# Kernel optimization log

Measured on AMD Instinct MI355X. Metric: run time of the kernel, lower is better.

The kernel has to match this reference:

```python
import jax, jax.numpy as jnp
import numpy as np

B, T, EMB, H = 4, 2048, 1024, 16
S = EMB // H


def setup_inputs() -> dict:
    key = jax.random.key(0)
    ks = jax.random.split(key, 7)
    x = jax.random.normal(ks[0], (B, T, EMB), dtype=jnp.float32)
    pad_amounts = jax.random.randint(ks[1], (B,), 0, 512, dtype=jnp.int64)
    Wk = jax.random.normal(ks[2], (S, S), dtype=jnp.float32) * (1.0 / np.sqrt(S))
    Wq = jax.random.normal(ks[3], (S, S), dtype=jnp.float32) * (1.0 / np.sqrt(S))
    Wv = jax.random.normal(ks[4], (S, S), dtype=jnp.float32) * (1.0 / np.sqrt(S))
    Wu = jax.random.normal(ks[5], (EMB, EMB), dtype=jnp.float32) * (1.0 / np.sqrt(EMB))
    bu = jax.random.normal(ks[6], (EMB,), dtype=jnp.float32) * 0.01
    return {"x": x, "Wk": Wk, "Wq": Wq, "Wv": Wv, "Wu": Wu, "bu": bu,
            "pad_amounts": pad_amounts}


def reference(x, Wk, Wq, Wv, Wu, bu, pad_amounts):
    b, t, e = x.shape
    h = H
    s = e // h
    xh = x.reshape(b, t, h, s)
    # torch Linear: y = x @ W.T (no bias for k/q/v)
    keys = jnp.einsum('bths,os->btho', xh, Wk)
    queries = jnp.einsum('bths,os->btho', xh, Wq)
    values = jnp.einsum('bths,os->btho', xh, Wv)
    # (b,t,h,s) -> (b*h,t,s)
    keys = keys.transpose(0, 2, 1, 3).reshape(b * h, t, s)
    queries = queries.transpose(0, 2, 1, 3).reshape(b * h, t, s)
    values = values.transpose(0, 2, 1, 3).reshape(b * h, t, s)
    scale = e ** 0.25
    queries = queries / scale
    keys = keys / scale
    dot = jnp.einsum('nqs,nks->nqk', queries, keys)  # (b*h, t, t)
    # Faithful to original bug: only the first b flat indices of b*h get masked.
    pad_full = jnp.concatenate([pad_amounts,
                                jnp.zeros(b * h - b, dtype=pad_amounts.dtype)])
    thresh = (t - pad_full)[:, None, None]  # (b*h,1,1); thresh=t -> no mask
    pos = jnp.arange(t)
    mask = (pos[None, :, None] >= thresh) & (pos[None, None, :] >= thresh)
    dot = jnp.where(mask, -jnp.inf, dot)
    att = jax.nn.softmax(dot, axis=2)
    out = jnp.einsum('nqk,nks->nqs', att, values)  # (b*h,t,s)
    out = out.reshape(b, h, t, s).transpose(0, 2, 1, 3).reshape(b, t, h * s)
    return out @ Wu.T + bu
```

## Files before the change

kernel.cpp:

```cpp
#include <hip/hip_runtime.h>


typedef float f32x4 __attribute__((ext_vector_type(4)));
typedef float f32x16 __attribute__((ext_vector_type(16)));
typedef _Float16 f16x2 __attribute__((ext_vector_type(2)));
typedef _Float16 f16x8 __attribute__((ext_vector_type(8)));
typedef unsigned u32x4 __attribute__((ext_vector_type(4)));

#define MFMA16(a, b, c) __builtin_amdgcn_mfma_f32_16x16x32_f16((a), (b), (c), 0, 0, 0)
#define MFMA32(a, b, c) __builtin_amdgcn_mfma_f32_32x32x16_f16((a), (b), (c), 0, 0, 0)

constexpr int Tn = 2048;
constexpr int Bn = 4;
constexpr int EMBn = 1024;
constexpr float NEG_INF = -3.0e38f;

__device__ __forceinline__ float exp2_hw(float x) {
  float r; asm("v_exp_f32 %0, %1" : "=v"(r) : "v"(x)); return r;
}
__device__ __forceinline__ unsigned pkrtz(float lo, float hi) {
  unsigned r; asm("v_cvt_pkrtz_f16_f32 %0, %1, %2" : "=v"(r) : "v"(lo), "v"(hi)); return r;
}
__device__ __forceinline__ unsigned pkadd(unsigned a, unsigned b) {
  unsigned r; asm("v_pk_add_f16 %0, %1, %2" : "=v"(r) : "v"(a), "v"(b)); return r;
}
__device__ __forceinline__ void permswap(unsigned& a, unsigned& b) {
  asm("v_permlane32_swap_b32 %0, %1" : "+v"(a), "+v"(b));
}

__global__ __launch_bounds__(256) void sa_prep(
    const float* __restrict__ Wk, const float* __restrict__ Wq,
    const float* __restrict__ Wv, const float* __restrict__ Wu,
    _Float16* __restrict__ w3, _Float16* __restrict__ wub) {
  int idx = blockIdx.x * 256 + threadIdx.x;
  const float rs = 0.21233046f;
  if (idx < 1048576) wub[idx] = (_Float16)Wu[idx];
  if (idx < 4096) {
    w3[idx]        = (_Float16)(Wk[idx] * rs);
    w3[4096 + idx] = (_Float16)(Wq[idx] * rs);
    w3[8192 + idx] = (_Float16)(Wv[idx]);
  }
}

__global__ __launch_bounds__(256) void sa_qkv(
    const float* __restrict__ x, const _Float16* __restrict__ w3,
    _Float16* __restrict__ Qb, _Float16* __restrict__ Kb, _Float16* __restrict__ Vt) {
  const int wave = threadIdx.x >> 6;
  const int lane = threadIdx.x & 63;
  const int g = lane >> 4, c = lane & 15;
  const int n = blockIdx.y, b = n >> 4, h = n & 15;
  const int t0 = blockIdx.x * 64 + wave * 16;

  f16x8 ax[2];
#pragma unroll
  for (int kk = 0; kk < 2; ++kk) {
    const float* xp = x + ((long)((b * Tn + t0 + c) * 16 + h)) * 64 + kk * 32 + g * 8;
    f32x4 u = *(const f32x4*)xp;
    f32x4 v = *(const f32x4*)(xp + 4);
    f16x8 a;
    a[0] = (_Float16)u[0]; a[1] = (_Float16)u[1]; a[2] = (_Float16)u[2]; a[3] = (_Float16)u[3];
    a[4] = (_Float16)v[0]; a[5] = (_Float16)v[1]; a[6] = (_Float16)v[2]; a[7] = (_Float16)v[3];
    ax[kk] = a;
  }

#pragma unroll
  for (int w = 0; w < 2; ++w) {
    _Float16* dst = w ? Qb : Kb;
#pragma unroll
    for (int ot = 0; ot < 4; ++ot) {
      f32x4 a_ = {0.f, 0.f, 0.f, 0.f};
#pragma unroll
      for (int kk = 0; kk < 2; ++kk) {
        f16x8 wf = *(const f16x8*)(w3 + w * 4096 + (ot * 16 + c) * 64 + kk * 32 + g * 8);
        a_ = MFMA16(ax[kk], wf, a_);
      }
#pragma unroll
      for (int r = 0; r < 4; ++r)
        dst[((long)n * Tn + t0 + g * 4 + r) * 64 + ot * 16 + c] = (_Float16)a_[r];
    }
  }

#pragma unroll
  for (int ot = 0; ot < 4; ++ot) {
    f32x4 a_ = {0.f, 0.f, 0.f, 0.f};
#pragma unroll
    for (int kk = 0; kk < 2; ++kk) {
      f16x8 wf = *(const f16x8*)(w3 + 8192 + (ot * 16 + c) * 64 + kk * 32 + g * 8);
      a_ = MFMA16(wf, ax[kk], a_);
    }
#pragma unroll
    for (int r = 0; r < 4; ++r)
      Vt[((long)n * 64 + ot * 16 + g * 4 + r) * Tn + t0 + c] = (_Float16)a_[r];
  }
}

__global__ __launch_bounds__(256, 2) void sa_flash(
    const _Float16* __restrict__ Qb, const _Float16* __restrict__ Kb,
    const _Float16* __restrict__ Vt, const int* __restrict__ pad32,
    _Float16* __restrict__ AO) {
  const int bid = blockIdx.x;
  const int n = (bid & 7) * 8 + (bid >> 6);
  const int qblk = (bid >> 3) & 7;
  const int tid = threadIdx.x;
  const int wave = tid >> 6;
  const int lane = tid & 63;
  const int ql = lane & 31;
  const int hi = lane >> 5;

  int thresh = Tn;
  if (n < Bn) {
    bool is64 = (pad32[1] == 0 && pad32[3] == 0);
    int pv = is64 ? pad32[2 * n] : pad32[n];
    thresh = Tn - pv;
  }

  const int qbase = qblk * 256 + wave * 64;
  const _Float16* Qh = Qb + (long)n * Tn * 64;
  const _Float16* Kh = Kb + (long)n * Tn * 64;
  const _Float16* Vh = Vt + (long)n * 64 * Tn;

  f16x8 bq[2][4];
#pragma unroll
  for (int qh = 0; qh < 2; ++qh) {
    const _Float16* qp = Qh + (long)(qbase + qh * 32 + ql) * 64 + hi * 8;
#pragma unroll
    for (int ks = 0; ks < 4; ++ks) bq[qh][ks] = *(const f16x8*)(qp + ks * 16);
  }

  __shared__ __align__(16) char smem[36864];

  const int sr = tid >> 2, sc = tid & 3;
  const _Float16* kgp = Kh + sr * 64 + sc * 8;
  const _Float16* vgp = Vh + (long)sr * Tn + sc * 8;
  char* kw = smem + sr * 144 + sc * 16;
  char* vw = smem + 18432 + sr * 144 + sc * 16;

  f32x16 o[2][2];
  f32x16 zf;
#pragma unroll
  for (int i = 0; i < 16; ++i) {
    o[0][0][i] = 0.f; o[0][1][i] = 0.f; o[1][0][i] = 0.f; o[1][1][i] = 0.f;
    zf[i] = 0.f;
  }
  float l0 = 0.f, l1 = 0.f;

  const bool qge0 = (qbase + ql) >= thresh;
  const bool qge1 = (qbase + 32 + ql) >= thresh;
  const bool qany = (qbase + 64) > thresh;

  {
    f16x8 k0 = *(const f16x8*)kgp;
    f16x8 k1 = *(const f16x8*)(kgp + 32);
    f16x8 v0 = *(const f16x8*)vgp;
    f16x8 v1 = *(const f16x8*)(vgp + 32);
    *(f16x8*)kw = k0;
    *(f16x8*)(kw + 64) = k1;
    *(f16x8*)vw = v0;
    *(f16x8*)(vw + 64) = v1;
  }
  __syncthreads();

  int cur = 0;
  for (int kb = 0; kb < Tn; kb += 64) {
    const int kbn = (kb + 64) & (Tn - 1);
    f16x8 kst0 = *(const f16x8*)(kgp + kbn * 64);
    f16x8 kst1 = *(const f16x8*)(kgp + kbn * 64 + 32);
    f16x8 vst0 = *(const f16x8*)(vgp + kbn);
    f16x8 vst1 = *(const f16x8*)(vgp + kbn + 32);

    const char* kbb = smem + cur * 9216;
    const char* vbb = smem + 18432 + cur * 9216;

#pragma unroll
    for (int sub = 0; sub < 2; ++sub) {
      const char* krow = kbb + (sub * 32 + ql) * 144 + hi * 16;
      f16x8 ka0 = *(const f16x8*)(krow);
      f16x8 ka1 = *(const f16x8*)(krow + 32);
      f16x8 ka2 = *(const f16x8*)(krow + 64);
      f16x8 ka3 = *(const f16x8*)(krow + 96);

      __builtin_amdgcn_s_setprio(1);
      f32x16 st0 = MFMA32(ka0, bq[0][0], zf);
      f32x16 st1 = MFMA32(ka0, bq[1][0], zf);
      st0 = MFMA32(ka1, bq[0][1], st0);
      st1 = MFMA32(ka1, bq[1][1], st1);
      st0 = MFMA32(ka2, bq[0][2], st0);
      st1 = MFMA32(ka2, bq[1][2], st1);
      st0 = MFMA32(ka3, bq[0][3], st0);
      st1 = MFMA32(ka3, bq[1][3], st1);
      __builtin_amdgcn_s_setprio(0);

      if (qany && (kb + sub * 32 + 32) > thresh) {
#pragma unroll
        for (int r = 0; r < 16; ++r) {
          int kr_ = kb + sub * 32 + (r & 3) + 8 * (r >> 2) + 4 * hi;
          if (kr_ >= thresh) {
            if (qge0) st0[r] = NEG_INF;
            if (qge1) st1[r] = NEG_INF;
          }
        }
      }

      const char* vrow0 = vbb + ql * 144 + sub * 64 + hi * 16;
      const char* vrow1 = vrow0 + 32 * 144;
      f16x8 va0 = *(const f16x8*)(vrow0);
      f16x8 va1 = *(const f16x8*)(vrow0 + 32);
      f16x8 va2 = *(const f16x8*)(vrow1);
      f16x8 va3 = *(const f16x8*)(vrow1 + 32);

#pragma unroll
      for (int qh = 0; qh < 2; ++qh) {
        const f32x16& stq = qh ? st1 : st0;
        float p[16];
#pragma unroll
        for (int r = 0; r < 16; ++r) p[r] = exp2_hw(stq[r]);

        unsigned pw[8], psum[2];
#pragma unroll
        for (int j = 0; j < 2; ++j) {
          unsigned a0 = pkrtz(p[j * 8 + 0], p[j * 8 + 1]);
          unsigned b0 = pkrtz(p[j * 8 + 4], p[j * 8 + 5]);
          unsigned a1 = pkrtz(p[j * 8 + 2], p[j * 8 + 3]);
          unsigned b1 = pkrtz(p[j * 8 + 6], p[j * 8 + 7]);
          psum[j] = pkadd(pkadd(a0, b0), pkadd(a1, b1));
          permswap(a0, b0);
          permswap(a1, b1);
          pw[j * 4 + 0] = a0; pw[j * 4 + 1] = a1;
          pw[j * 4 + 2] = b0; pw[j * 4 + 3] = b1;
        }
        {
          f16x2 ph = __builtin_bit_cast(f16x2, pkadd(psum[0], psum[1]));
          if (qh) l1 += (float)ph[0] + (float)ph[1];
          else    l0 += (float)ph[0] + (float)ph[1];
        }
        u32x4 u0 = {pw[0], pw[1], pw[2], pw[3]};
        u32x4 u1 = {pw[4], pw[5], pw[6], pw[7]};
        f16x8 pb0 = __builtin_bit_cast(f16x8, u0);
        f16x8 pb1 = __builtin_bit_cast(f16x8, u1);

        __builtin_amdgcn_s_setprio(1);
        o[qh][0] = MFMA32(va0, pb0, o[qh][0]);
        o[qh][0] = MFMA32(va1, pb1, o[qh][0]);
        o[qh][1] = MFMA32(va2, pb0, o[qh][1]);
        o[qh][1] = MFMA32(va3, pb1, o[qh][1]);
        __builtin_amdgcn_s_setprio(0);
      }
    }

    char* kwd = kw + (cur ^ 1) * 9216;
    char* vwd = vw + (cur ^ 1) * 9216;
    *(f16x8*)kwd = kst0;
    *(f16x8*)(kwd + 64) = kst1;
    *(f16x8*)vwd = vst0;
    *(f16x8*)(vwd + 64) = vst1;
    __syncthreads();
    cur ^= 1;
  }

  float lf0 = l0 + __shfl_xor(l0, 32, 64);
  float lf1 = l1 + __shfl_xor(l1, 32, 64);
  float linv0 = 1.0f / lf0;
  float linv1 = 1.0f / lf1;

  const int bb = n >> 4, hh = n & 15;
  const int qr = lane >> 3, s0 = (lane & 7) * 8;
  _Float16* my = (_Float16*)(smem + wave * 8192);
#pragma unroll
  for (int qh = 0; qh < 2; ++qh) {
    float linv = qh ? linv1 : linv0;
    _Float16* myq = my + qh * 2048;
#pragma unroll
    for (int stile = 0; stile < 2; ++stile) {
#pragma unroll
      for (int r = 0; r < 16; r += 2) {
        unsigned wv = pkrtz(o[qh][stile][r] * linv, o[qh][stile][r + 1] * linv);
        int s = stile * 32 + (r & 3) + 8 * (r >> 2) + 4 * hi;
        *(unsigned*)(myq + ql * 64 + (s ^ ((ql & 7) << 3))) = wv;
      }
    }
  }
  asm volatile("s_waitcnt lgkmcnt(0)" ::: "memory");

#pragma unroll
  for (int qh = 0; qh < 2; ++qh) {
    _Float16* myq = my + qh * 2048;
#pragma unroll
    for (int j = 0; j < 4; ++j) {
      int q = j * 8 + qr;
      f16x8 vv = *(const f16x8*)(myq + q * 64 + (s0 ^ ((q & 7) << 3)));
      *(f16x8*)(AO + ((long)(bb * Tn + qbase + qh * 32 + q)) * EMBn + hh * 64 + s0) = vv;
    }
  }
}

__global__ __launch_bounds__(256, 4) void sa_oproj(
    const _Float16* __restrict__ A, const _Float16* __restrict__ WuB,
    const float* __restrict__ bu, float* __restrict__ Y) {
  const int bid = blockIdx.x;
  const int xcd = bid & 7;
  const int j = bid >> 3;
  const int nstrip = j & 15;
  const int mblk = xcd * 8 + (j >> 4);
  const int tid = threadIdx.x;
  const int wave = tid >> 6;
  const int lane = tid & 63;
  const int ql = lane & 31;
  const int hi = lane >> 5;
  const int mbase = mblk * 128 + wave * 32;
  const int nbase = nstrip * 64;

  __shared__ __align__(16) char bsm[18432];
  const int sr = tid >> 3, sc = tid & 7;
  const _Float16* wg0 = WuB + (long)(nbase + sr) * 1024 + sc * 8;
  const _Float16* wg1 = WuB + (long)(nbase + sr + 32) * 1024 + sc * 8;
  char* ww0 = bsm + sr * 144 + sc * 16;
  char* ww1 = bsm + (sr + 32) * 144 + sc * 16;

  const _Float16* ap = A + (long)(mbase + ql) * 1024 + hi * 8;

  f32x16 acc[2];
#pragma unroll
  for (int i = 0; i < 16; ++i) { acc[0][i] = 0.f; acc[1][i] = 0.f; }

  {
    f16x8 w0 = *(const f16x8*)wg0;
    f16x8 w1 = *(const f16x8*)wg1;
    *(f16x8*)ww0 = w0;
    *(f16x8*)ww1 = w1;
  }
  __syncthreads();

  int cur = 0;
  for (int kb = 0; kb < 1024; kb += 64) {
    const int kbn = (kb + 64) & 1023;
    f16x8 wn0 = *(const f16x8*)(wg0 + kbn);
    f16x8 wn1 = *(const f16x8*)(wg1 + kbn);

    f16x8 af[4];
#pragma unroll
    for (int ks = 0; ks < 4; ++ks) af[ks] = *(const f16x8*)(ap + kb + ks * 16);

    const char* bbase = bsm + cur * 9216;
#pragma unroll
    for (int nt = 0; nt < 2; ++nt) {
      const char* brow = bbase + (nt * 32 + ql) * 144;
#pragma unroll
      for (int ks = 0; ks < 4; ++ks) {
        f16x8 bf = *(const f16x8*)(brow + (ks * 2 + hi) * 16);
        acc[nt] = MFMA32(af[ks], bf, acc[nt]);
      }
    }

    *(f16x8*)(ww0 + (cur ^ 1) * 9216) = wn0;
    *(f16x8*)(ww1 + (cur ^ 1) * 9216) = wn1;
    __syncthreads();
    cur ^= 1;
  }

#pragma unroll
  for (int nt = 0; nt < 2; ++nt) {
    float bias = bu[nbase + nt * 32 + ql];
#pragma unroll
    for (int r = 0; r < 16; ++r) {
      int mrow = mbase + (r & 3) + 8 * (r >> 2) + 4 * hi;
      Y[(long)mrow * 1024 + nbase + nt * 32 + ql] = acc[nt][r] + bias;
    }
  }
}

extern "C" void kernel_launch(void* const* d_in, const int* in_sizes, int n_in,
                              void* d_out, int out_size, void* d_ws, size_t ws_size,
                              hipStream_t stream) {
  const float* x  = (const float*)d_in[0];
  const float* Wk = (const float*)d_in[1];
  const float* Wq = (const float*)d_in[2];
  const float* Wv = (const float*)d_in[3];
  const float* Wu = (const float*)d_in[4];
  const float* bu = (const float*)d_in[5];
  const int* pad  = (const int*)d_in[6];
  float* Y = (float*)d_out;

  _Float16* ws  = (_Float16*)d_ws;
  _Float16* w3  = ws;
  _Float16* wub = ws + 16384;
  _Float16* Qb  = ws + 16384 + 1048576;
  _Float16* Kb  = Qb + 8388608;
  _Float16* Vt  = Kb + 8388608;
  _Float16* AO  = Vt + 8388608;

  sa_prep<<<4096, 256, 0, stream>>>(Wk, Wq, Wv, Wu, w3, wub);
  sa_qkv<<<dim3(32, 64), 256, 0, stream>>>(x, w3, Qb, Kb, Vt);
  sa_flash<<<dim3(512), 256, 0, stream>>>(Qb, Kb, Vt, pad, AO);
  sa_oproj<<<dim3(1024), 256, 0, stream>>>(AO, wub, bu, Y);
}
```

Baseline: 148.0 us.

## Stream K/V tiles into LDS with direct global-to-LDS loads and XOR swizzle

```diff
diff --git a/kernel.cpp b/kernel.cpp
--- a/kernel.cpp
+++ b/kernel.cpp
@@ -26,6 +26,11 @@
 }
 __device__ __forceinline__ void permswap(unsigned& a, unsigned& b) {
   asm("v_permlane32_swap_b32 %0, %1" : "+v"(a), "+v"(b));
+}
+__device__ __forceinline__ void glds16(const void* g, void* l) {
+  __builtin_amdgcn_global_load_lds(
+      (const __attribute__((address_space(1))) unsigned*)g,
+      (__attribute__((address_space(3))) unsigned*)l, 16, 0, 0);
 }
 
 __global__ __launch_bounds__(256) void sa_prep(
@@ -127,13 +132,12 @@
     for (int ks = 0; ks < 4; ++ks) bq[qh][ks] = *(const f16x8*)(qp + ks * 16);
   }
 
-  __shared__ __align__(16) char smem[36864];
-
-  const int sr = tid >> 2, sc = tid & 3;
-  const _Float16* kgp = Kh + sr * 64 + sc * 8;
-  const _Float16* vgp = Vh + (long)sr * Tn + sc * 8;
-  char* kw = smem + sr * 144 + sc * 16;
-  char* vw = smem + 18432 + sr * 144 + sc * 16;
+  __shared__ __align__(16) char smem[32768];
+
+  const int srow = wave * 16 + (lane >> 3);
+  const int sswz = ((lane & 7) ^ (lane >> 3)) * 8;
+  const _Float16* ksrc = Kh + (long)srow * 64 + sswz;
+  const _Float16* vsrc = Vh + (long)srow * Tn + sswz;
 
   f32x16 o[2][2];
   f32x16 zf;
@@ -147,37 +151,40 @@
   const bool qge0 = (qbase + ql) >= thresh;
   const bool qge1 = (qbase + 32 + ql) >= thresh;
   const bool qany = (qbase + 64) > thresh;
+  const int sw = ql & 7;
 
   {
-    f16x8 k0 = *(const f16x8*)kgp;
-    f16x8 k1 = *(const f16x8*)(kgp + 32);
-    f16x8 v0 = *(const f16x8*)vgp;
-    f16x8 v1 = *(const f16x8*)(vgp + 32);
-    *(f16x8*)kw = k0;
-    *(f16x8*)(kw + 64) = k1;
-    *(f16x8*)vw = v0;
-    *(f16x8*)(vw + 64) = v1;
+    char* kd = smem + wave * 2048;
+    char* vd = smem + 16384 + wave * 2048;
+    glds16(ksrc, kd);
+    glds16(ksrc + 512, kd + 1024);
+    glds16(vsrc, vd);
+    glds16(vsrc + 8 * Tn, vd + 1024);
   }
   __syncthreads();
 
   int cur = 0;
   for (int kb = 0; kb < Tn; kb += 64) {
     const int kbn = (kb + 64) & (Tn - 1);
-    f16x8 kst0 = *(const f16x8*)(kgp + kbn * 64);
-    f16x8 kst1 = *(const f16x8*)(kgp + kbn * 64 + 32);
-    f16x8 vst0 = *(const f16x8*)(vgp + kbn);
-    f16x8 vst1 = *(const f16x8*)(vgp + kbn + 32);
-
-    const char* kbb = smem + cur * 9216;
-    const char* vbb = smem + 18432 + cur * 9216;
+    {
+      char* kd = smem + (cur ^ 1) * 8192 + wave * 2048;
+      char* vd = smem + 16384 + (cur ^ 1) * 8192 + wave * 2048;
+      glds16(ksrc + kbn * 64, kd);
+      glds16(ksrc + kbn * 64 + 512, kd + 1024);
+      glds16(vsrc + kbn, vd);
+      glds16(vsrc + kbn + 8 * Tn, vd + 1024);
+    }
+
+    const char* kbb = smem + cur * 8192;
+    const char* vbb = smem + 16384 + cur * 8192;
 
 #pragma unroll
     for (int sub = 0; sub < 2; ++sub) {
-      const char* krow = kbb + (sub * 32 + ql) * 144 + hi * 16;
-      f16x8 ka0 = *(const f16x8*)(krow);
-      f16x8 ka1 = *(const f16x8*)(krow + 32);
-      f16x8 ka2 = *(const f16x8*)(krow + 64);
-      f16x8 ka3 = *(const f16x8*)(krow + 96);
+      const char* krow = kbb + (sub * 32 + ql) * 128;
+      f16x8 ka0 = *(const f16x8*)(krow + (((0 + hi) ^ sw) * 16));
+      f16x8 ka1 = *(const f16x8*)(krow + (((2 + hi) ^ sw) * 16));
+      f16x8 ka2 = *(const f16x8*)(krow + (((4 + hi) ^ sw) * 16));
+      f16x8 ka3 = *(const f16x8*)(krow + (((6 + hi) ^ sw) * 16));
 
       __builtin_amdgcn_s_setprio(1);
       f32x16 st0 = MFMA32(ka0, bq[0][0], zf);
@@ -201,12 +208,12 @@
         }
       }
 
-      const char* vrow0 = vbb + ql * 144 + sub * 64 + hi * 16;
-      const char* vrow1 = vrow0 + 32 * 144;
-      f16x8 va0 = *(const f16x8*)(vrow0);
-      f16x8 va1 = *(const f16x8*)(vrow0 + 32);
-      f16x8 va2 = *(const f16x8*)(vrow1);
-      f16x8 va3 = *(const f16x8*)(vrow1 + 32);
+      const char* vrow0 = vbb + ql * 128;
+      const char* vrow1 = vbb + (ql + 32) * 128;
+      f16x8 va0 = *(const f16x8*)(vrow0 + (((sub * 4 + hi) ^ sw) * 16));
+      f16x8 va1 = *(const f16x8*)(vrow0 + (((sub * 4 + 2 + hi) ^ sw) * 16));
+      f16x8 va2 = *(const f16x8*)(vrow1 + (((sub * 4 + hi) ^ sw) * 16));
+      f16x8 va3 = *(const f16x8*)(vrow1 + (((sub * 4 + 2 + hi) ^ sw) * 16));
 
 #pragma unroll
       for (int qh = 0; qh < 2; ++qh) {
@@ -247,12 +254,6 @@
       }
     }
 
-    char* kwd = kw + (cur ^ 1) * 9216;
-    char* vwd = vw + (cur ^ 1) * 9216;
-    *(f16x8*)kwd = kst0;
-    *(f16x8*)(kwd + 64) = kst1;
-    *(f16x8*)vwd = vst0;
-    *(f16x8*)(vwd + 64) = vst1;
     __syncthreads();
     cur ^= 1;
   }
```

Measured after the change: 148.6 us. Within noise of the previous version (+0.4%).
